# Kernel optimization log

Measured on AMD Instinct MI355X. Metric: run time of the kernel, lower is better.

## Reference

```python
import jax, jax.numpy as jnp
import numpy as np

T, B, D, H, L = 512, 64, 800, 400, 3  # D == 2*H so all layers share weight shapes


def setup_inputs() -> dict:
    key = jax.random.key(0)
    ks = jax.random.split(key, 10)
    s = 0.02
    x = jax.random.normal(ks[0], (T, B, D), dtype=jnp.float32)
    masks = jnp.ones((T, B, 1), dtype=jnp.float32)
    fW = jax.random.normal(ks[1], (L, 3 * H, D + H), dtype=jnp.float32) * s
    fb = jnp.zeros((L, 3 * H), dtype=jnp.float32)
    bW = jax.random.normal(ks[2], (L, 3 * H, D + H), dtype=jnp.float32) * s
    bb = jnp.zeros((L, 3 * H), dtype=jnp.float32)
    f_init = jax.random.normal(ks[3], (L, 2, H), dtype=jnp.float32) * s
    b_init = jax.random.normal(ks[4], (L, 2, H), dtype=jnp.float32) * s
    pW = jax.random.normal(ks[5], (L - 1, 2 * H, 2 * H), dtype=jnp.float32) * s
    pb = jnp.zeros((L - 1, 2 * H), dtype=jnp.float32)
    return {"x": x, "masks": masks, "fW": fW, "fb": fb, "bW": bW, "bb": bb,
            "f_init": f_init, "b_init": b_init, "pW": pW, "pb": pb}


def _run_dir(W, b, init, xs, ms, reverse):
    # xs: [T,B,Din], ms: [T,B,1]; 3-gate coupled-input LSTM cell
    batch = xs.shape[1]
    h0 = jnp.broadcast_to(init[0], (batch, H))
    c0 = jnp.broadcast_to(init[1], (batch, H))

    def step(carry, inp):
        h, c = carry
        xt, mt = inp
        g = jnp.concatenate([xt, h], axis=1) @ W.T + b  # [B,3H]
        i, j, o = jnp.split(g, 3, axis=1)
        i = jax.nn.sigmoid(i)
        c = mt * ((1.0 - i) * c + i * jnp.tanh(j))
        h = mt * (jnp.tanh(c) * jax.nn.sigmoid(o))
        return (h, c), h

    (hT, cT), ys = jax.lax.scan(step, (h0, c0), (xs, ms), reverse=reverse)
    return ys, hT, cT


def reference(x, masks, fW, fb, bW, bb, f_init, b_init, pW, pb):
    inp = x
    h_n, c_n = [], []
    for layer in range(L):
        f_out, fh, fc = _run_dir(fW[layer], fb[layer], f_init[layer], inp, masks, False)
        b_out, bh, bc = _run_dir(bW[layer], bb[layer], b_init[layer], inp, masks, True)
        h_n += [fh, bh]
        c_n += [fc, bc]
        out = jnp.concatenate([f_out, b_out], axis=2)  # [T,B,2H]
        if layer > 0:
            gates = jax.nn.sigmoid(out @ pW[layer - 1].T + pb[layer - 1])
            out = gates * out + (1.0 - gates) * inp
        inp = out
    h_n = jnp.stack(h_n, 0)  # [2L,B,H]
    c_n = jnp.stack(c_n, 0)
    return out, h_n, c_n
```

## Files before the change

### kernel.cpp

```cpp
#include <hip/hip_runtime.h>

typedef __attribute__((ext_vector_type(8))) short short8;
typedef __attribute__((ext_vector_type(4))) float f32x4;
typedef unsigned short u16;
typedef unsigned int u32;

#define T_LEN 512
#define BATCH 64
#define HID 400
#define GATES 1200
#define DIN 800
#define KTOT 1200
#define WSTRIDE 1216
#define HSTRIDE 416
#define NKK 38
#define FLAG_STRIDE 32

__device__ __forceinline__ u16 f2bf(float f) {
    u32 u = __builtin_bit_cast(u32, f);
    u += 0x7fffu + ((u >> 16) & 1u);
    return (u16)(u >> 16);
}
__device__ __forceinline__ float sigmoidf_(float x) { return 1.f / (1.f + expf(-x)); }

__global__ void cast_f32_bf16(const float* __restrict__ in, u16* __restrict__ out, int n) {
    for (int i = blockIdx.x * blockDim.x + threadIdx.x; i < n; i += gridDim.x * blockDim.x)
        out[i] = f2bf(in[i]);
}

__global__ void cast_W(const float* __restrict__ fW, const float* __restrict__ bW,
                       u16* __restrict__ W_bf, int layer) {
    const int n = 2 * GATES * WSTRIDE;
    for (int i = blockIdx.x * blockDim.x + threadIdx.x; i < n; i += gridDim.x * blockDim.x) {
        int d = i / (GATES * WSTRIDE);
        int rem = i - d * (GATES * WSTRIDE);
        int r = rem / WSTRIDE;
        int k = rem - r * WSTRIDE;
        const float* src = (d ? bW : fW) + (size_t)layer * GATES * KTOT;
        W_bf[i] = (k < KTOT) ? f2bf(src[(size_t)r * KTOT + k]) : (u16)0;
    }
}

__global__ void init_states(const float* __restrict__ f_init, const float* __restrict__ b_init,
                            u16* __restrict__ h_bf, int layer) {
    const int n = 2 * 2 * BATCH * HSTRIDE;
    for (int i = blockIdx.x * blockDim.x + threadIdx.x; i < n; i += gridDim.x * blockDim.x) {
        int d = i / (2 * BATCH * HSTRIDE);
        int rem = i - d * (2 * BATCH * HSTRIDE);
        int buf = rem / (BATCH * HSTRIDE);
        int rem2 = rem - buf * (BATCH * HSTRIDE);
        int k = rem2 % HSTRIDE;
        const float* src = (d ? b_init : f_init) + layer * 2 * HID;
        h_bf[i] = (k < HID && buf == 0) ? f2bf(src[k]) : (u16)0;
    }
}

__device__ __forceinline__ void load_x25(const u16* p, short8* d) {
    asm volatile(
        "global_load_dwordx4 %0,  %25, off\n\t"
        "global_load_dwordx4 %1,  %25, off offset:64\n\t"
        "global_load_dwordx4 %2,  %25, off offset:128\n\t"
        "global_load_dwordx4 %3,  %25, off offset:192\n\t"
        "global_load_dwordx4 %4,  %25, off offset:256\n\t"
        "global_load_dwordx4 %5,  %25, off offset:320\n\t"
        "global_load_dwordx4 %6,  %25, off offset:384\n\t"
        "global_load_dwordx4 %7,  %25, off offset:448\n\t"
        "global_load_dwordx4 %8,  %25, off offset:512\n\t"
        "global_load_dwordx4 %9,  %25, off offset:576\n\t"
        "global_load_dwordx4 %10, %25, off offset:640\n\t"
        "global_load_dwordx4 %11, %25, off offset:704\n\t"
        "global_load_dwordx4 %12, %25, off offset:768\n\t"
        "global_load_dwordx4 %13, %25, off offset:832\n\t"
        "global_load_dwordx4 %14, %25, off offset:896\n\t"
        "global_load_dwordx4 %15, %25, off offset:960\n\t"
        "global_load_dwordx4 %16, %25, off offset:1024\n\t"
        "global_load_dwordx4 %17, %25, off offset:1088\n\t"
        "global_load_dwordx4 %18, %25, off offset:1152\n\t"
        "global_load_dwordx4 %19, %25, off offset:1216\n\t"
        "global_load_dwordx4 %20, %25, off offset:1280\n\t"
        "global_load_dwordx4 %21, %25, off offset:1344\n\t"
        "global_load_dwordx4 %22, %25, off offset:1408\n\t"
        "global_load_dwordx4 %23, %25, off offset:1472\n\t"
        "global_load_dwordx4 %24, %25, off offset:1536"
        : "=&v"(d[0]), "=&v"(d[1]), "=&v"(d[2]), "=&v"(d[3]), "=&v"(d[4]),
          "=&v"(d[5]), "=&v"(d[6]), "=&v"(d[7]), "=&v"(d[8]), "=&v"(d[9]),
          "=&v"(d[10]), "=&v"(d[11]), "=&v"(d[12]), "=&v"(d[13]), "=&v"(d[14]),
          "=&v"(d[15]), "=&v"(d[16]), "=&v"(d[17]), "=&v"(d[18]), "=&v"(d[19]),
          "=&v"(d[20]), "=&v"(d[21]), "=&v"(d[22]), "=&v"(d[23]), "=&v"(d[24])
        : "v"(p)
        : "memory");
}

__global__ __launch_bounds__(192, 1) void lstm_persist(
    const u16* __restrict__ x_bf,
    const u16* __restrict__ W_bf,
    const float* __restrict__ fb_l,
    const float* __restrict__ bb_l,
    const float* __restrict__ masks,
    const float* __restrict__ finit,
    const float* __restrict__ binit,
    u16* __restrict__ h_bf,
    float* __restrict__ c_end,
    float* __restrict__ raw,
    int* __restrict__ flagsL)
{
    const int dir = blockIdx.z;
    const int pl  = blockIdx.x;
    const int bb  = blockIdx.y * 16;
    const int tid = threadIdx.x;
    const int lane = tid & 63, gate = tid >> 6;
    const int l15 = lane & 15, hi = lane >> 4;
    const int gid = dir * 4 + blockIdx.y;

    int* myflag = flagsL + (gid * 25 + pl) * FLAG_STRIDE;
    const int fl = (lane < 25) ? lane : 24;
    const int* pollp = flagsL + (gid * 25 + fl) * FLAG_STRIDE;

    __shared__ u16 Wlds[NKK * 192 * 8];
    __shared__ float gsm[3][16][16];
    __shared__ float c_lds[16][16];

    {
        const u16* Wsrc = W_bf + (size_t)dir * GATES * WSTRIDE;
        const int pr = gate * HID + pl * 16 + l15;
        const int k0 = 8 * hi;
        for (int kk = 0; kk < NKK; ++kk)
            *(short8*)&Wlds[(size_t)(kk * 192 + tid) * 8] =
                *(const short8*)(Wsrc + (size_t)pr * WSTRIDE + kk * 32 + k0);
    }

    const float* init = dir ? binit : finit;
    for (int i = tid; i < 256; i += 192)
        c_lds[i >> 4][i & 15] = init[HID + pl * 16 + (i & 15)];

    const int prow = gate * HID + pl * 16 + l15;
    const float bval = (dir ? bb_l : fb_l)[prow];
    const u16* wfrag = &Wlds[(size_t)tid * 8];

    const int bi_c = (tid >> 3) & 15;

    __syncthreads();

    short8 xc[25];
    {
        const int t0 = dir ? (T_LEN - 1) : 0;
        load_x25(x_bf + (size_t)(t0 * BATCH + bb + l15) * DIN + 8 * hi, xc);
        asm volatile("s_waitcnt vmcnt(0)" ::: "memory");
        __builtin_amdgcn_sched_barrier(0);
    }

    for (int tf = 0; tf < T_LEN; ++tf) {
        const int t = dir ? (T_LEN - 1 - tf) : tf;

        if (tf > 0) {
            while (__hip_atomic_load(pollp, __ATOMIC_RELAXED, __HIP_MEMORY_SCOPE_AGENT) < tf)
                __builtin_amdgcn_s_sleep(1);
            asm volatile("s_waitcnt vmcnt(0)" ::: "memory");
            __builtin_amdgcn_sched_barrier(0);
        }

        const u16* Hrow = h_bf + (size_t)((dir * 2 + (tf & 1)) * BATCH + bb + l15) * HSTRIDE + 8 * hi;
        const float* maddr = masks + t * BATCH + bb + bi_c;
        short8 hf[13];
        float mreg;
        asm volatile(
            "global_load_dwordx4 %0,  %14, off sc0 sc1\n\t"
            "global_load_dwordx4 %1,  %14, off offset:64 sc0 sc1\n\t"
            "global_load_dwordx4 %2,  %14, off offset:128 sc0 sc1\n\t"
            "global_load_dwordx4 %3,  %14, off offset:192 sc0 sc1\n\t"
            "global_load_dwordx4 %4,  %14, off offset:256 sc0 sc1\n\t"
            "global_load_dwordx4 %5,  %14, off offset:320 sc0 sc1\n\t"
            "global_load_dwordx4 %6,  %14, off offset:384 sc0 sc1\n\t"
            "global_load_dwordx4 %7,  %14, off offset:448 sc0 sc1\n\t"
            "global_load_dwordx4 %8,  %14, off offset:512 sc0 sc1\n\t"
            "global_load_dwordx4 %9,  %14, off offset:576 sc0 sc1\n\t"
            "global_load_dwordx4 %10, %14, off offset:640 sc0 sc1\n\t"
            "global_load_dwordx4 %11, %14, off offset:704 sc0 sc1\n\t"
            "global_load_dwordx4 %12, %14, off offset:768 sc0 sc1\n\t"
            "global_load_dword   %13, %15, off"
            : "=&v"(hf[0]), "=&v"(hf[1]), "=&v"(hf[2]), "=&v"(hf[3]), "=&v"(hf[4]),
              "=&v"(hf[5]), "=&v"(hf[6]), "=&v"(hf[7]), "=&v"(hf[8]), "=&v"(hf[9]),
              "=&v"(hf[10]), "=&v"(hf[11]), "=&v"(hf[12]), "=&v"(mreg)
            : "v"(Hrow), "v"(maddr)
            : "memory");

        f32x4 acc = {bval, bval, bval, bval};
#pragma unroll
        for (int kk = 0; kk < 25; ++kk)
            acc = __builtin_amdgcn_mfma_f32_16x16x32_bf16(
                xc[kk], *(const short8*)(wfrag + (size_t)kk * 1536), acc, 0, 0, 0);

        asm volatile("s_waitcnt vmcnt(0)" ::: "memory");
        __builtin_amdgcn_sched_barrier(0);
#pragma unroll
        for (int kk = 0; kk < 13; ++kk)
            acc = __builtin_amdgcn_mfma_f32_16x16x32_bf16(
                hf[kk], *(const short8*)(wfrag + (size_t)(25 + kk) * 1536), acc, 0, 0, 0);

#pragma unroll
        for (int j = 0; j < 4; ++j) gsm[gate][hi * 4 + j][l15] = acc[j];
        __syncthreads();

        if (tid < 128) {
            const int bi = tid >> 3, cp = (tid & 7) * 2;
            const int bg = bb + bi;
            const float m = mreg;
            float h2[2];
#pragma unroll
            for (int q = 0; q < 2; ++q) {
                const int c = cp + q;
                float ig = sigmoidf_(gsm[0][bi][c]);
                float jg = tanhf(gsm[1][bi][c]);
                float og = sigmoidf_(gsm[2][bi][c]);
                float cold = c_lds[bi][c];
                float cn = m * ((1.f - ig) * cold + ig * jg);
                c_lds[bi][c] = cn;
                h2[q] = m * (tanhf(cn) * og);
            }
            u32 hp = (u32)f2bf(h2[0]) | ((u32)f2bf(h2[1]) << 16);
            u16* hdst = h_bf + (size_t)((dir * 2 + ((tf + 1) & 1)) * BATCH + bg) * HSTRIDE + pl * 16 + cp;
            asm volatile("global_store_dword %[a], %[d], off sc0 sc1"
                         :: [a] "v"(hdst), [d] "v"(hp) : "memory");
            float2 rv = make_float2(h2[0], h2[1]);
            *(float2*)(raw + ((size_t)t * BATCH + bg) * (2 * HID) + dir * HID + pl * 16 + cp) = rv;
        }

        __syncthreads();
        if (tf < T_LEN - 1) {
            if (tid == 0)
                __hip_atomic_store(myflag, tf + 1, __ATOMIC_RELAXED, __HIP_MEMORY_SCOPE_AGENT);
            const int tn = dir ? (T_LEN - 2 - tf) : tf + 1;
            load_x25(x_bf + (size_t)(tn * BATCH + bb + l15) * DIN + 8 * hi, xc);
        }
    }

    if (tid < 128) {
        const int bi = tid >> 3, cp = (tid & 7) * 2;
        const int bg = bb + bi;
        float* cd = c_end + (size_t)(dir * BATCH + bg) * HID + pl * 16 + cp;
        cd[0] = c_lds[bi][cp];
        cd[1] = c_lds[bi][cp + 1];
    }
}

__global__ void save_states(const float* __restrict__ raw, const float* __restrict__ c_ws,
                            float* __restrict__ out, int layer) {
    const int n = 2 * BATCH * HID;
    for (int i = blockIdx.x * blockDim.x + threadIdx.x; i < n; i += gridDim.x * blockDim.x) {
        int d = i / (BATCH * HID);
        int rem = i - d * (BATCH * HID);
        int b = rem / HID;
        int k = rem - b * HID;
        int t = d ? 0 : (T_LEN - 1);
        float h = raw[((size_t)t * BATCH + b) * (2 * HID) + d * HID + k];
        size_t base = (size_t)T_LEN * BATCH * (2 * HID);
        size_t idx = ((size_t)(2 * layer + d) * BATCH + b) * HID + k;
        out[base + idx] = h;
        out[base + (size_t)2 * 3 * BATCH * HID + idx] = c_ws[d * (BATCH * HID) + b * HID + k];
    }
}

__global__ __launch_bounds__(256) void highway_gemm(
    const u16* __restrict__ A, const u16* __restrict__ Bw, const float* __restrict__ pb,
    float* __restrict__ Rcur, const float* __restrict__ Iprev)
{
    const int m0 = blockIdx.x * 128;
    const int n0 = blockIdx.y * 128;
    const int tid = threadIdx.x, lane = tid & 63, wave = tid >> 6;
    const int wy = wave >> 1, wx = wave & 1;
    const int l15 = lane & 15, hi = lane >> 4;
    const short8 zero8 = {};

    f32x4 acc[4][4] = {};
    const int arow0 = m0 + wy * 64 + l15;
    const int brow0 = n0 + wx * 64 + l15;

    for (int kk = 0; kk < 25; ++kk) {
        const int k0 = kk * 32 + 8 * hi;
        short8 a[4], b[4];
#pragma unroll
        for (int mf = 0; mf < 4; ++mf)
            a[mf] = *(const short8*)(A + (size_t)(arow0 + mf * 16) * DIN + k0);
#pragma unroll
        for (int nf = 0; nf < 4; ++nf) {
            int br = brow0 + nf * 16;
            b[nf] = (br < DIN) ? *(const short8*)(Bw + (size_t)br * DIN + k0) : zero8;
        }
#pragma unroll
        for (int mf = 0; mf < 4; ++mf)
#pragma unroll
            for (int nf = 0; nf < 4; ++nf)
                acc[mf][nf] = __builtin_amdgcn_mfma_f32_16x16x32_bf16(a[mf], b[nf], acc[mf][nf], 0, 0, 0);
    }

#pragma unroll
    for (int mf = 0; mf < 4; ++mf)
#pragma unroll
        for (int nf = 0; nf < 4; ++nf)
#pragma unroll
            for (int j = 0; j < 4; ++j) {
                int row = m0 + wy * 64 + mf * 16 + hi * 4 + j;
                int col = n0 + wx * 64 + nf * 16 + l15;
                if (col < DIN) {
                    float g = sigmoidf_(acc[mf][nf][j] + pb[col]);
                    size_t off = (size_t)row * DIN + col;
                    Rcur[off] = g * Rcur[off] + (1.f - g) * Iprev[off];
                }
            }
}

extern "C" void kernel_launch(void* const* d_in, const int* in_sizes, int n_in,
                              void* d_out, int out_size, void* d_ws, size_t ws_size,
                              hipStream_t stream) {
    const float* x      = (const float*)d_in[0];
    const float* masks  = (const float*)d_in[1];
    const float* fW     = (const float*)d_in[2];
    const float* fb     = (const float*)d_in[3];
    const float* bW     = (const float*)d_in[4];
    const float* bb     = (const float*)d_in[5];
    const float* f_init = (const float*)d_in[6];
    const float* b_init = (const float*)d_in[7];
    const float* pW     = (const float*)d_in[8];
    const float* pb     = (const float*)d_in[9];
    float* out = (float*)d_out;

    char* ws = (char*)d_ws;
    float* R0   = (float*)(ws + 0);
    float* R1   = (float*)(ws + 104857600);
    u16* x_bf   = (u16*)(ws + 209715200);
    u16* W_bf   = (u16*)(ws + 262144000);
    u16* pW_bf  = (u16*)(ws + 267980800);
    u16* h_bf   = (u16*)(ws + 269260800);
    float* c_ws = (float*)(ws + 269473792);
    int* bar    = (int*)(ws + 269678592);
    const int N_TB = T_LEN * BATCH * DIN;
    const int FLAGS_PER_LAYER = 8 * 25 * FLAG_STRIDE;

    hipMemsetAsync(bar, 0, 3 * FLAGS_PER_LAYER * sizeof(int), stream);

    for (int layer = 0; layer < 3; ++layer) {
        float* raw = (layer == 0) ? R0 : (layer == 1) ? R1 : out;
        const float* inp_f32 = (layer == 0) ? x : (layer == 1) ? R0 : R1;

        cast_f32_bf16<<<4096, 256, 0, stream>>>(inp_f32, x_bf, N_TB);
        cast_W<<<4096, 256, 0, stream>>>(fW, bW, W_bf, layer);
        init_states<<<(2 * 2 * BATCH * HSTRIDE + 255) / 256, 256, 0, stream>>>(f_init, b_init, h_bf, layer);

        lstm_persist<<<dim3(25, 4, 2), 192, 0, stream>>>(
            x_bf, W_bf, fb + layer * GATES, bb + layer * GATES, masks,
            f_init + layer * 2 * HID, b_init + layer * 2 * HID,
            h_bf, c_ws, raw, bar + layer * FLAGS_PER_LAYER);

        save_states<<<200, 256, 0, stream>>>(raw, c_ws, out, layer);

        if (layer > 0) {
            cast_f32_bf16<<<4096, 256, 0, stream>>>(raw, x_bf, N_TB);
            cast_f32_bf16<<<2048, 256, 0, stream>>>(pW + (size_t)(layer - 1) * DIN * DIN, pW_bf, DIN * DIN);
            highway_gemm<<<dim3(256, 7), 256, 0, stream>>>(
                x_bf, pW_bf, pb + (layer - 1) * DIN, raw, inp_f32);
        }
    }
}
```

Baseline: 5.661 ms.

## Add runtime-probed same-XCD fast sync path with per-wave flags for persistent LSTM

Blocks are relaunched as a 1D grid so that each batch/direction group (bidx&7) is expected to land on one XCD. At startup a timed token-exchange probe checks whether plain stores are visible to sc0 loads across the group. If every block sees them, a templated fast loop runs: h-state loads, stores and flag traffic drop the system-scope sc1 bit and the flag poll loop no longer sleeps. Otherwise the old coherent path is used. Each of the two elementwise waves now publishes its own flag, which removes the per-step __syncthreads before signalling. The risks are the startup probe cost, dependence on how hardware places blocks onto XCDs, and subtle memory-ordering assumptions in the fast path.

```diff
diff --git a/kernel.cpp b/kernel.cpp
--- a/kernel.cpp
+++ b/kernel.cpp
@@ -4,6 +4,7 @@
 typedef __attribute__((ext_vector_type(4))) float f32x4;
 typedef unsigned short u16;
 typedef unsigned int u32;
+typedef unsigned long long u64;
 
 #define T_LEN 512
 #define BATCH 64
@@ -12,9 +13,13 @@
 #define DIN 800
 #define KTOT 1200
 #define WSTRIDE 1216
-#define HSTRIDE 416
+#define HSTRIDE 448
 #define NKK 38
-#define FLAG_STRIDE 32
+
+#define ARR_OFF   12800
+#define TOK_OFF   19200
+#define VOTE_OFF  25600
+#define SYNC_INTS 32000
 
 __device__ __forceinline__ u16 f2bf(float f) {
     u32 u = __builtin_bit_cast(u32, f);
@@ -91,78 +96,31 @@
         : "memory");
 }
 
-__global__ __launch_bounds__(192, 1) void lstm_persist(
-    const u16* __restrict__ x_bf,
-    const u16* __restrict__ W_bf,
-    const float* __restrict__ fb_l,
-    const float* __restrict__ bb_l,
-    const float* __restrict__ masks,
-    const float* __restrict__ finit,
-    const float* __restrict__ binit,
-    u16* __restrict__ h_bf,
-    float* __restrict__ c_end,
-    float* __restrict__ raw,
-    int* __restrict__ flagsL)
-{
-    const int dir = blockIdx.z;
-    const int pl  = blockIdx.x;
-    const int bb  = blockIdx.y * 16;
-    const int tid = threadIdx.x;
-    const int lane = tid & 63, gate = tid >> 6;
-    const int l15 = lane & 15, hi = lane >> 4;
-    const int gid = dir * 4 + blockIdx.y;
-
-    int* myflag = flagsL + (gid * 25 + pl) * FLAG_STRIDE;
-    const int fl = (lane < 25) ? lane : 24;
-    const int* pollp = flagsL + (gid * 25 + fl) * FLAG_STRIDE;
-
-    __shared__ u16 Wlds[NKK * 192 * 8];
-    __shared__ float gsm[3][16][16];
-    __shared__ float c_lds[16][16];
-
-    {
-        const u16* Wsrc = W_bf + (size_t)dir * GATES * WSTRIDE;
-        const int pr = gate * HID + pl * 16 + l15;
-        const int k0 = 8 * hi;
-        for (int kk = 0; kk < NKK; ++kk)
-            *(short8*)&Wlds[(size_t)(kk * 192 + tid) * 8] =
-                *(const short8*)(Wsrc + (size_t)pr * WSTRIDE + kk * 32 + k0);
-    }
-
-    const float* init = dir ? binit : finit;
-    for (int i = tid; i < 256; i += 192)
-        c_lds[i >> 4][i & 15] = init[HID + pl * 16 + (i & 15)];
-
-    const int prow = gate * HID + pl * 16 + l15;
-    const float bval = (dir ? bb_l : fb_l)[prow];
-    const u16* wfrag = &Wlds[(size_t)tid * 8];
-
-    const int bi_c = (tid >> 3) & 15;
-
-    __syncthreads();
-
-    short8 xc[25];
-    {
-        const int t0 = dir ? (T_LEN - 1) : 0;
-        load_x25(x_bf + (size_t)(t0 * BATCH + bb + l15) * DIN + 8 * hi, xc);
-        asm volatile("s_waitcnt vmcnt(0)" ::: "memory");
-        __builtin_amdgcn_sched_barrier(0);
-    }
-
-    for (int tf = 0; tf < T_LEN; ++tf) {
-        const int t = dir ? (T_LEN - 1 - tf) : tf;
-
-        if (tf > 0) {
-            while (__hip_atomic_load(pollp, __ATOMIC_RELAXED, __HIP_MEMORY_SCOPE_AGENT) < tf)
-                __builtin_amdgcn_s_sleep(1);
-            asm volatile("s_waitcnt vmcnt(0)" ::: "memory");
-            __builtin_amdgcn_sched_barrier(0);
-        }
-
-        const u16* Hrow = h_bf + (size_t)((dir * 2 + (tf & 1)) * BATCH + bb + l15) * HSTRIDE + 8 * hi;
-        const float* maddr = masks + t * BATCH + bb + bi_c;
-        short8 hf[13];
-        float mreg;
+template<bool FAST>
+__device__ __forceinline__ void hload13t(const u16* Hrow, const float* maddr,
+                                         short8* hf, float& mreg) {
+    if constexpr (FAST) {
+        asm volatile(
+            "global_load_dwordx4 %0,  %14, off sc0\n\t"
+            "global_load_dwordx4 %1,  %14, off offset:64 sc0\n\t"
+            "global_load_dwordx4 %2,  %14, off offset:128 sc0\n\t"
+            "global_load_dwordx4 %3,  %14, off offset:192 sc0\n\t"
+            "global_load_dwordx4 %4,  %14, off offset:256 sc0\n\t"
+            "global_load_dwordx4 %5,  %14, off offset:320 sc0\n\t"
+            "global_load_dwordx4 %6,  %14, off offset:384 sc0\n\t"
+            "global_load_dwordx4 %7,  %14, off offset:448 sc0\n\t"
+            "global_load_dwordx4 %8,  %14, off offset:512 sc0\n\t"
+            "global_load_dwordx4 %9,  %14, off offset:576 sc0\n\t"
+            "global_load_dwordx4 %10, %14, off offset:640 sc0\n\t"
+            "global_load_dwordx4 %11, %14, off offset:704 sc0\n\t"
+            "global_load_dwordx4 %12, %14, off offset:768 sc0\n\t"
+            "global_load_dword   %13, %15, off"
+            : "=&v"(hf[0]), "=&v"(hf[1]), "=&v"(hf[2]), "=&v"(hf[3]), "=&v"(hf[4]),
+              "=&v"(hf[5]), "=&v"(hf[6]), "=&v"(hf[7]), "=&v"(hf[8]), "=&v"(hf[9]),
+              "=&v"(hf[10]), "=&v"(hf[11]), "=&v"(hf[12]), "=&v"(mreg)
+            : "v"(Hrow), "v"(maddr)
+            : "memory");
+    } else {
         asm volatile(
             "global_load_dwordx4 %0,  %14, off sc0 sc1\n\t"
             "global_load_dwordx4 %1,  %14, off offset:64 sc0 sc1\n\t"
@@ -183,6 +141,83 @@
               "=&v"(hf[10]), "=&v"(hf[11]), "=&v"(hf[12]), "=&v"(mreg)
             : "v"(Hrow), "v"(maddr)
             : "memory");
+    }
+}
+
+template<bool FAST>
+__device__ __forceinline__ void hstore1t(u16* p, u32 v) {
+    if constexpr (FAST)
+        asm volatile("global_store_dword %0, %1, off" :: "v"(p), "v"(v) : "memory");
+    else
+        asm volatile("global_store_dword %0, %1, off sc0 sc1" :: "v"(p), "v"(v) : "memory");
+}
+
+template<bool FAST>
+__device__ __forceinline__ void flagstore_t(int* p, int v) {
+    if constexpr (FAST)
+        asm volatile("global_store_dword %0, %1, off" :: "v"(p), "v"(v) : "memory");
+    else
+        __hip_atomic_store(p, v, __ATOMIC_RELAXED, __HIP_MEMORY_SCOPE_AGENT);
+}
+
+template<bool FAST>
+__device__ __forceinline__ int flagpoll_t(const int* p) {
+    if constexpr (FAST) {
+        int v;
+        asm volatile("global_load_dword %0, %1, off sc0\n\ts_waitcnt vmcnt(0)"
+                     : "=v"(v) : "v"(p) : "memory");
+        return v;
+    } else {
+        return __hip_atomic_load(p, __ATOMIC_RELAXED, __HIP_MEMORY_SCOPE_AGENT);
+    }
+}
+
+__device__ __forceinline__ int ld_sc0p(const int* p) {
+    int v;
+    asm volatile("global_load_dword %0, %1, off sc0\n\ts_waitcnt vmcnt(0)"
+                 : "=v"(v) : "v"(p) : "memory");
+    return v;
+}
+__device__ __forceinline__ void st_plainp(int* p, int v) {
+    asm volatile("global_store_dword %0, %1, off\n\ts_waitcnt vmcnt(0)"
+                 :: "v"(p), "v"(v) : "memory");
+}
+
+template<bool FAST>
+__device__ __forceinline__ void lstm_loop(
+    const u16* __restrict__ x_bf, const float* __restrict__ masks,
+    u16* __restrict__ h_bf, float* __restrict__ raw,
+    int* sfbase, int* myfA, const int* pollp,
+    const u16* wfrag, float bval,
+    float (*gsm)[16][16], float (*c_lds)[16],
+    int dir, int bb, int pl, int tid, int lane, int gate, int l15, int hi, int bi_c)
+{
+    short8 xc[25];
+    {
+        const int t0 = dir ? (T_LEN - 1) : 0;
+        load_x25(x_bf + (size_t)(t0 * BATCH + bb + l15) * DIN + 8 * hi, xc);
+        asm volatile("s_waitcnt vmcnt(0)" ::: "memory");
+        __builtin_amdgcn_sched_barrier(0);
+    }
+
+    for (int tf = 0; tf < T_LEN; ++tf) {
+        const int t = dir ? (T_LEN - 1 - tf) : tf;
+
+        if (tf > 0) {
+            int v = flagpoll_t<FAST>(pollp);
+            while (v < tf) {
+                if constexpr (!FAST) __builtin_amdgcn_s_sleep(1);
+                v = flagpoll_t<FAST>(pollp);
+            }
+            asm volatile("s_waitcnt vmcnt(0)" ::: "memory");
+            __builtin_amdgcn_sched_barrier(0);
+        }
+
+        const u16* Hrow = h_bf + (size_t)((dir * 2 + (tf & 1)) * BATCH + bb + l15) * HSTRIDE + 8 * hi;
+        const float* maddr = masks + t * BATCH + bb + bi_c;
+        short8 hf[13];
+        float mreg;
+        hload13t<FAST>(Hrow, maddr, hf, mreg);
 
         f32x4 acc = {bval, bval, bval, bval};
 #pragma unroll
@@ -219,20 +254,126 @@
             }
             u32 hp = (u32)f2bf(h2[0]) | ((u32)f2bf(h2[1]) << 16);
             u16* hdst = h_bf + (size_t)((dir * 2 + ((tf + 1) & 1)) * BATCH + bg) * HSTRIDE + pl * 16 + cp;
-            asm volatile("global_store_dword %[a], %[d], off sc0 sc1"
-                         :: [a] "v"(hdst), [d] "v"(hp) : "memory");
+            hstore1t<FAST>(hdst, hp);
             float2 rv = make_float2(h2[0], h2[1]);
             *(float2*)(raw + ((size_t)t * BATCH + bg) * (2 * HID) + dir * HID + pl * 16 + cp) = rv;
+
+            if (tf < T_LEN - 1) {
+                asm volatile("s_waitcnt vmcnt(0)" ::: "memory");
+                if ((tid & 63) == 0)
+                    flagstore_t<FAST>(myfA + (tid >> 6) * 32, tf + 1);
+            }
         }
 
-        __syncthreads();
         if (tf < T_LEN - 1) {
-            if (tid == 0)
-                __hip_atomic_store(myflag, tf + 1, __ATOMIC_RELAXED, __HIP_MEMORY_SCOPE_AGENT);
             const int tn = dir ? (T_LEN - 2 - tf) : tf + 1;
             load_x25(x_bf + (size_t)(tn * BATCH + bb + l15) * DIN + 8 * hi, xc);
         }
     }
+}
+
+__global__ __launch_bounds__(192, 1) void lstm_persist(
+    const u16* __restrict__ x_bf,
+    const u16* __restrict__ W_bf,
+    const float* __restrict__ fb_l,
+    const float* __restrict__ bb_l,
+    const float* __restrict__ masks,
+    const float* __restrict__ finit,
+    const float* __restrict__ binit,
+    u16* __restrict__ h_bf,
+    float* __restrict__ c_end,
+    float* __restrict__ raw,
+    int* __restrict__ syncL)
+{
+    const int bidx = blockIdx.x;
+    const int gid = bidx & 7;
+    const int pl  = bidx >> 3;
+    const int dir = gid >> 2;
+    const int bb  = (gid & 3) * 16;
+    const int tid = threadIdx.x;
+    const int lane = tid & 63, gate = tid >> 6;
+    const int l15 = lane & 15, hi = lane >> 4;
+
+    int* sfbase = syncL + (size_t)gid * 50 * 32;
+    int* myfA   = sfbase + (pl * 2) * 32;
+    const int pollidx = (lane < 25) ? lane * 2 : (lane < 50 ? (lane - 25) * 2 + 1 : 49);
+    const int* pollp = sfbase + pollidx * 32;
+    int* arrb  = syncL + ARR_OFF + gid * 25 * 32;
+    int* tokb  = syncL + TOK_OFF + gid * 25 * 32;
+    int* voteb = syncL + VOTE_OFF + gid * 25 * 32;
+
+    __shared__ int mode_sh;
+
+    if (tid == 0)
+        __hip_atomic_store(arrb + pl * 32, 1, __ATOMIC_RELAXED, __HIP_MEMORY_SCOPE_AGENT);
+    if (tid < 64) {
+        const int al = (lane < 25) ? lane : 24;
+        while (__hip_atomic_load(arrb + al * 32, __ATOMIC_RELAXED, __HIP_MEMORY_SCOPE_AGENT) == 0)
+            __builtin_amdgcn_s_sleep(1);
+    }
+    __syncthreads();
+
+    bool okAll = true;
+    for (int r = 1; r <= 3; ++r) {
+        if (tid == 0) st_plainp(tokb + pl * 32, r);
+        if (tid < 64) {
+            const int tl = (lane < 25) ? lane : 24;
+            u64 t0 = __builtin_amdgcn_s_memrealtime();
+            const u64 TH = (r == 1) ? 1000 : 300;
+            bool seen = false;
+            while (true) {
+                int v = ld_sc0p(tokb + tl * 32);
+                if (__all(v == r)) { seen = true; break; }
+                if (__builtin_amdgcn_s_memrealtime() - t0 > TH) break;
+            }
+            okAll = okAll && seen;
+        }
+        __syncthreads();
+    }
+    if (tid == 0)
+        __hip_atomic_store(voteb + pl * 32, okAll ? 2 : 1, __ATOMIC_RELAXED, __HIP_MEMORY_SCOPE_AGENT);
+    if (tid < 64) {
+        const int vl = (lane < 25) ? lane : 24;
+        int v;
+        do {
+            v = __hip_atomic_load(voteb + vl * 32, __ATOMIC_RELAXED, __HIP_MEMORY_SCOPE_AGENT);
+            if (v == 0) __builtin_amdgcn_s_sleep(1);
+        } while (v == 0);
+        if (lane == 0) mode_sh = __all(v == 2) ? 1 : 0;
+    }
+    __syncthreads();
+    const bool fastm = (mode_sh == 1);
+
+    __shared__ u16 Wlds[NKK * 192 * 8];
+    __shared__ float gsm[3][16][16];
+    __shared__ float c_lds[16][16];
+
+    {
+        const u16* Wsrc = W_bf + (size_t)dir * GATES * WSTRIDE;
+        const int pr = gate * HID + pl * 16 + l15;
+        const int k0 = 8 * hi;
+        for (int kk = 0; kk < NKK; ++kk)
+            *(short8*)&Wlds[(size_t)(kk * 192 + tid) * 8] =
+                *(const short8*)(Wsrc + (size_t)pr * WSTRIDE + kk * 32 + k0);
+    }
+
+    const float* init = dir ? binit : finit;
+    for (int i = tid; i < 256; i += 192)
+        c_lds[i >> 4][i & 15] = init[HID + pl * 16 + (i & 15)];
+
+    const int prow = gate * HID + pl * 16 + l15;
+    const float bval = (dir ? bb_l : fb_l)[prow];
+    const u16* wfrag = &Wlds[(size_t)tid * 8];
+    const int bi_c = (tid >> 3) & 15;
+
+    __syncthreads();
+
+    if (fastm)
+        lstm_loop<true>(x_bf, masks, h_bf, raw, sfbase, myfA, pollp, wfrag, bval,
+                        gsm, c_lds, dir, bb, pl, tid, lane, gate, l15, hi, bi_c);
+    else
+        lstm_loop<false>(x_bf, masks, h_bf, raw, sfbase, myfA, pollp, wfrag, bval,
+                         gsm, c_lds, dir, bb, pl, tid, lane, gate, l15, hi, bi_c);
 
     if (tid < 128) {
         const int bi = tid >> 3, cp = (tid & 7) * 2;
@@ -331,12 +472,11 @@
     u16* W_bf   = (u16*)(ws + 262144000);
     u16* pW_bf  = (u16*)(ws + 267980800);
     u16* h_bf   = (u16*)(ws + 269260800);
-    float* c_ws = (float*)(ws + 269473792);
-    int* bar    = (int*)(ws + 269678592);
+    float* c_ws = (float*)(ws + 269490176);
+    int* syncb  = (int*)(ws + 269694976);
     const int N_TB = T_LEN * BATCH * DIN;
-    const int FLAGS_PER_LAYER = 8 * 25 * FLAG_STRIDE;
-
-    hipMemsetAsync(bar, 0, 3 * FLAGS_PER_LAYER * sizeof(int), stream);
+
+    hipMemsetAsync(syncb, 0, 3 * SYNC_INTS * sizeof(int), stream);
 
     for (int layer = 0; layer < 3; ++layer) {
         float* raw = (layer == 0) ? R0 : (layer == 1) ? R1 : out;
@@ -346,10 +486,10 @@
         cast_W<<<4096, 256, 0, stream>>>(fW, bW, W_bf, layer);
         init_states<<<(2 * 2 * BATCH * HSTRIDE + 255) / 256, 256, 0, stream>>>(f_init, b_init, h_bf, layer);
 
-        lstm_persist<<<dim3(25, 4, 2), 192, 0, stream>>>(
+        lstm_persist<<<200, 192, 0, stream>>>(
             x_bf, W_bf, fb + layer * GATES, bb + layer * GATES, masks,
             f_init + layer * 2 * HID, b_init + layer * 2 * HID,
-            h_bf, c_ws, raw, bar + layer * FLAGS_PER_LAYER);
+            h_bf, c_ws, raw, syncb + layer * SYNC_INTS);
 
         save_states<<<200, 256, 0, stream>>>(raw, c_ws, out, layer);
 
```

New measurement: 6.637 ms. +17.2%, slower.

## Use per-wave completion flags and pipelined spin polling in persistent LSTM

Applied to the files above, without the earlier changes.

Each block now publishes two flags, one per storing wave, so a wave signals right after its own h store drains. This drops the block-wide __syncthreads before the flag store. The poll loop takes out the s_sleep and keeps two outstanding flag loads in flight to cut wake-up latency. Consumers poll 50 flags across lanes. The trade is more flag traffic and busier spinning, plus a subtle reliance on vmcnt ordering for correctness, since the syncthreads that previously separated LDS c_lds/gsm reuse is gone.

```diff
diff --git a/kernel.cpp b/kernel.cpp
--- a/kernel.cpp
+++ b/kernel.cpp
@@ -4,6 +4,7 @@
 typedef __attribute__((ext_vector_type(4))) float f32x4;
 typedef unsigned short u16;
 typedef unsigned int u32;
+typedef unsigned long long u64;
 
 #define T_LEN 512
 #define BATCH 64
@@ -15,6 +16,7 @@
 #define HSTRIDE 416
 #define NKK 38
 #define FLAG_STRIDE 32
+#define FLAGS_PER_LAYER (8 * 50 * FLAG_STRIDE)
 
 __device__ __forceinline__ u16 f2bf(float f) {
     u32 u = __builtin_bit_cast(u32, f);
@@ -112,9 +114,10 @@
     const int l15 = lane & 15, hi = lane >> 4;
     const int gid = dir * 4 + blockIdx.y;
 
-    int* myflag = flagsL + (gid * 25 + pl) * FLAG_STRIDE;
-    const int fl = (lane < 25) ? lane : 24;
-    const int* pollp = flagsL + (gid * 25 + fl) * FLAG_STRIDE;
+    int* sfbase = flagsL + (size_t)gid * 50 * FLAG_STRIDE;
+    int* myflag = sfbase + (pl * 2) * FLAG_STRIDE;
+    const int pollidx = (lane < 25) ? lane * 2 : (lane < 50 ? (lane - 25) * 2 + 1 : 49);
+    const int* pollp = sfbase + pollidx * FLAG_STRIDE;
 
     __shared__ u16 Wlds[NKK * 192 * 8];
     __shared__ float gsm[3][16][16];
@@ -153,10 +156,29 @@
         const int t = dir ? (T_LEN - 1 - tf) : tf;
 
         if (tf > 0) {
-            while (__hip_atomic_load(pollp, __ATOMIC_RELAXED, __HIP_MEMORY_SCOPE_AGENT) < tf)
-                __builtin_amdgcn_s_sleep(1);
-            asm volatile("s_waitcnt vmcnt(0)" ::: "memory");
+            int va, vb;
+            asm volatile("global_load_dword %0, %1, off sc0 sc1\n\t"
+                         "s_waitcnt vmcnt(0)"
+                         : "=v"(va) : "v"(pollp) : "memory");
             __builtin_amdgcn_sched_barrier(0);
+            if (!__all(va >= tf)) {
+                asm volatile("global_load_dword %0, %1, off sc0 sc1"
+                             : "=v"(va) : "v"(pollp) : "memory");
+                while (true) {
+                    asm volatile("global_load_dword %0, %1, off sc0 sc1"
+                                 : "=v"(vb) : "v"(pollp) : "memory");
+                    asm volatile("s_waitcnt vmcnt(1)" ::: "memory");
+                    __builtin_amdgcn_sched_barrier(0);
+                    if (__all(va >= tf)) break;
+                    asm volatile("global_load_dword %0, %1, off sc0 sc1"
+                                 : "=v"(va) : "v"(pollp) : "memory");
+                    asm volatile("s_waitcnt vmcnt(1)" ::: "memory");
+                    __builtin_amdgcn_sched_barrier(0);
+                    if (__all(vb >= tf)) break;
+                }
+                asm volatile("s_waitcnt vmcnt(0)" ::: "memory");
+                __builtin_amdgcn_sched_barrier(0);
+            }
         }
 
         const u16* Hrow = h_bf + (size_t)((dir * 2 + (tf & 1)) * BATCH + bb + l15) * HSTRIDE + 8 * hi;
@@ -219,16 +241,22 @@
             }
             u32 hp = (u32)f2bf(h2[0]) | ((u32)f2bf(h2[1]) << 16);
             u16* hdst = h_bf + (size_t)((dir * 2 + ((tf + 1) & 1)) * BATCH + bg) * HSTRIDE + pl * 16 + cp;
-            asm volatile("global_store_dword %[a], %[d], off sc0 sc1"
-                         :: [a] "v"(hdst), [d] "v"(hp) : "memory");
             float2 rv = make_float2(h2[0], h2[1]);
-            *(float2*)(raw + ((size_t)t * BATCH + bg) * (2 * HID) + dir * HID + pl * 16 + cp) = rv;
-        }
-
-        __syncthreads();
+            u64 rp = __builtin_bit_cast(u64, rv);
+            float* rdst = raw + ((size_t)t * BATCH + bg) * (2 * HID) + dir * HID + pl * 16 + cp;
+            asm volatile("global_store_dword %0, %1, off sc0 sc1\n\t"
+                         "global_store_dwordx2 %2, %3, off"
+                         :: "v"(hdst), "v"(hp), "v"(rdst), "v"(rp)
+                         : "memory");
+            if (tf < T_LEN - 1) {
+                asm volatile("s_waitcnt vmcnt(1)" ::: "memory");
+                if ((tid & 63) == 0)
+                    __hip_atomic_store(myflag + (tid >> 6) * FLAG_STRIDE, tf + 1,
+                                       __ATOMIC_RELAXED, __HIP_MEMORY_SCOPE_AGENT);
+            }
+        }
+
         if (tf < T_LEN - 1) {
-            if (tid == 0)
-                __hip_atomic_store(myflag, tf + 1, __ATOMIC_RELAXED, __HIP_MEMORY_SCOPE_AGENT);
             const int tn = dir ? (T_LEN - 2 - tf) : tf + 1;
             load_x25(x_bf + (size_t)(tn * BATCH + bb + l15) * DIN + 8 * hi, xc);
         }
@@ -334,7 +362,6 @@
     float* c_ws = (float*)(ws + 269473792);
     int* bar    = (int*)(ws + 269678592);
     const int N_TB = T_LEN * BATCH * DIN;
-    const int FLAGS_PER_LAYER = 8 * 25 * FLAG_STRIDE;
 
     hipMemsetAsync(bar, 0, 3 * FLAGS_PER_LAYER * sizeof(int), stream);
 
```

New measurement: 6.205 ms. +9.6%, slower.
